# Kernel tuning notes

Hardware: AMD Instinct MI355X
Metric: run time of the kernel (lower is better)

The kernel has to match this reference:

```python
import jax, jax.numpy as jnp
import numpy as np

N_NODES = 50000
N_EDGES = 800000
D = 128
L = 3
BN_EPS = 1e-5


def _l2norm(x):
    # torch F.normalize(p=2, dim=-1): x / max(||x||, 1e-12)
    n = jnp.linalg.norm(x, axis=-1, keepdims=True)
    return x / jnp.maximum(n, 1e-12)


def setup_inputs() -> dict:
    key = jax.random.key(0)
    ks = jax.random.split(key, 5)
    x = jax.random.normal(ks[0], (N_NODES, D), dtype=jnp.float32)
    edge_index = jax.random.randint(ks[1], (2, N_EDGES), 0, N_NODES, dtype=jnp.int64)
    # stacked per-layer params; Linear stored as [in, out] (y = x @ W + b)
    W1 = jax.random.normal(ks[2], (L, D, D), dtype=jnp.float32) * 0.05
    W2 = jax.random.normal(ks[3], (L, D, D), dtype=jnp.float32) * 0.05
    b1 = jnp.zeros((L, D), jnp.float32)
    b2 = jnp.zeros((L, D), jnp.float32)
    gamma = jnp.ones((L, D), jnp.float32)
    beta = jnp.zeros((L, D), jnp.float32)
    eps = jnp.zeros((L,), jnp.float32)
    return {"x": x, "edge_index": edge_index, "W1": W1, "b1": b1,
            "gamma": gamma, "beta": beta, "W2": W2, "b2": b2, "eps": eps}


def _gin_layer(x, src, dst, W1, b1, g, be, W2, b2, eps):
    # message + scatter-add aggregation: sum_j x_j -> node i
    agg = jax.ops.segment_sum(x[src], dst, num_segments=N_NODES)
    # update(): L2 normalize aggregated messages
    agg = _l2norm(agg)
    # eps-weighted residual on L2-normalized root features
    out = agg + (1.0 + eps) * _l2norm(x)
    # MLP: Linear -> BatchNorm1d (training stats) -> ReLU -> Linear
    h = out @ W1 + b1
    mu = jnp.mean(h, axis=0)
    var = jnp.mean(jnp.square(h - mu), axis=0)  # biased var (torch BN training)
    h = g * (h - mu) * jax.lax.rsqrt(var + BN_EPS) + be
    h = jax.nn.relu(h)
    return h @ W2 + b2


def reference(x, edge_index, W1, b1, gamma, beta, W2, b2, eps):
    src, dst = edge_index[0], edge_index[1]
    for i in range(L):
        x = _gin_layer(x, src, dst, W1[i], b1[i], gamma[i], beta[i], W2[i], b2[i], eps[i])
        if i != L - 1:
            x = jax.nn.relu(x)
    return x
```

## Files before the change

kernel.cpp:

```cpp
#include <hip/hip_runtime.h>
#include <hip/hip_bf16.h>

#define N_NODES 50000
#define N_EDGES 800000
#define D 128
#define L_LAYERS 3
#define BN_EPS 1e-5f
#define NBUK 196
#define BIN_CHUNK 4096
#define NBIN_BLOCKS 196
#define BSTRIDE 5120
#define CSTRIDE 5376
#define AROW 68
#define NPART 8
#define PADOFF (N_NODES << 8)

typedef __attribute__((ext_vector_type(8))) short short8;
typedef __attribute__((ext_vector_type(4))) float floatx4;
typedef __attribute__((ext_vector_type(4))) unsigned short ushort4v;

__device__ __forceinline__ unsigned short f2bf(float f) {
    unsigned u = __builtin_bit_cast(unsigned, f);
    u += 0x7FFFu + ((u >> 16) & 1u);
    return (unsigned short)(u >> 16);
}
__device__ __forceinline__ float bf2f(unsigned short h) {
    unsigned u = ((unsigned)h) << 16;
    return __builtin_bit_cast(float, u);
}
__device__ __forceinline__ float bf2f_lo(unsigned p) {
    return __builtin_bit_cast(float, p << 16);
}
__device__ __forceinline__ float bf2f_hi(unsigned p) {
    return __builtin_bit_cast(float, p & 0xFFFF0000u);
}

__device__ __forceinline__ int edge_at(const void* ei, const int* flag64, long long i) {
    if (*flag64) return (int)((const long long*)ei)[i];
    return ((const int*)ei)[i];
}

__global__ __launch_bounds__(256) void prep_kernel(const float* __restrict__ x,
        const void* __restrict__ ei, int* __restrict__ flag,
        const float* __restrict__ W1, const float* __restrict__ W2,
        short* __restrict__ Wp, unsigned short* __restrict__ xb,
        unsigned* __restrict__ zreg, int zwords) {
    int bid = blockIdx.x;
    int t = threadIdx.x;
    if (bid == 0) {
        __shared__ int nz;
        if (t == 0) nz = 0;
        __syncthreads();
        if (((const int*)ei)[2 * t + 1] != 0) atomicAdd(&nz, 1);
        __syncthreads();
        if (t == 0) *flag = (nz == 0) ? 1 : 0;
        for (int i = t; i < zwords; i += 256) zreg[i] = 0u;
        if (t < 64) ((unsigned*)(xb + (size_t)N_NODES * D))[t] = 0u;
    } else if (bid <= 48) {
        int tid = (bid - 1) * 256 + t;
        int mat = tid >> 11;
        int t2 = tid & 2047;
        int kt = t2 >> 9;
        int nt = (t2 >> 6) & 7;
        int lane = t2 & 63;
        const float* W = (mat < 3) ? (W1 + (size_t)mat * D * D)
                                   : (W2 + (size_t)(mat - 3) * D * D);
        int kbase = kt * 32 + (lane >> 4) * 8;
        int n = nt * 16 + (lane & 15);
        short8 frag;
        #pragma unroll
        for (int j = 0; j < 8; j++) frag[j] = (short)f2bf(W[(kbase + j) * D + n]);
        *(short8*)(Wp + (size_t)mat * D * D + (size_t)t2 * 8) = frag;
    } else {
        long long i = (long long)((bid - 49) * 256 + t) * 4;
        float4 v = *(const float4*)(x + i);
        ushort4v o;
        o.x = f2bf(v.x); o.y = f2bf(v.y); o.z = f2bf(v.z); o.w = f2bf(v.w);
        *(ushort4v*)(xb + i) = o;
    }
}

__global__ __launch_bounds__(256) void bin_kernel(const void* __restrict__ ei,
        const int* __restrict__ flag64, int* __restrict__ bucketCursor,
        unsigned* __restrict__ binned) {
    __shared__ int lhist[NBUK];
    __shared__ int gbase[NBUK];
    int t = threadIdx.x;
    for (int i = t; i < NBUK; i += 256) lhist[i] = 0;
    __syncthreads();

    int e0 = blockIdx.x * BIN_CHUNK;
    unsigned w[BIN_CHUNK / 256];
    short bkt[BIN_CHUNK / 256];
    short lidx[BIN_CHUNK / 256];
    #pragma unroll
    for (int i = 0; i < BIN_CHUNK / 256; i++) {
        int e = e0 + t + i * 256;
        if (e < N_EDGES) {
            int s = edge_at(ei, flag64, e);
            int d = edge_at(ei, flag64, (long long)N_EDGES + e);
            int b = d >> 8;
            w[i] = ((unsigned)s << 8) | (unsigned)(d & 255);
            bkt[i] = (short)b;
            lidx[i] = (short)atomicAdd(&lhist[b], 1);
        } else {
            bkt[i] = -1;
        }
    }
    __syncthreads();
    for (int i = t; i < NBUK; i += 256) {
        int c = lhist[i];
        gbase[i] = i * BSTRIDE + (c ? atomicAdd(&bucketCursor[i], c) : 0);
    }
    __syncthreads();
    #pragma unroll
    for (int i = 0; i < BIN_CHUNK / 256; i++) {
        if (bkt[i] >= 0)
            binned[gbase[bkt[i]] + (int)lidx[i]] = w[i];
    }
}

__global__ __launch_bounds__(256) void csr_build_kernel(const unsigned* __restrict__ binned,
        const int* __restrict__ bucketCursor, int* __restrict__ rowptr,
        int* __restrict__ bucketEnd, int* __restrict__ csr) {
    __shared__ int ls[256];
    __shared__ int lhist[256];
    __shared__ int lcur[256];
    int b = blockIdx.x, t = threadIdx.x;
    int n = bucketCursor[b];
    const unsigned* src = binned + (size_t)b * BSTRIDE;

    lhist[t] = 0;
    __syncthreads();
    for (int i = t; i < n; i += 256)
        atomicAdd(&lhist[src[i] & 255u], 1);
    __syncthreads();
    int c = lhist[t];
    int pc = (c + 3) & ~3;
    ls[t] = pc;
    __syncthreads();
    for (int off = 1; off < 256; off <<= 1) {
        int u = (t >= off) ? ls[t - off] : 0;
        __syncthreads();
        ls[t] += u;
        __syncthreads();
    }
    int excl = ls[t] - pc;
    int base = b * CSTRIDE;
    int dst = b * 256 + t;
    if (dst <= N_NODES) rowptr[dst] = base + excl;
    if (t == 0) bucketEnd[b] = base + ls[255];
    lcur[t] = excl;
    __syncthreads();
    for (int i = t; i < n; i += 256) {
        unsigned wv = src[i];
        int pos = atomicAdd(&lcur[wv & 255u], 1);
        csr[base + pos] = (int)(wv & 0xFFFFFF00u);
    }
    __syncthreads();
    for (int i = lcur[t]; i < excl + pc; i++)
        csr[base + i] = PADOFF;
}

__global__ __launch_bounds__(256, 8) void gather_gemm1_kernel(
        const unsigned short* __restrict__ xb,
        const int* __restrict__ rowptr, const int* __restrict__ csr,
        const int* __restrict__ bucketEnd,
        const float* __restrict__ epsArr, int layer,
        const short* __restrict__ Wp, const float* __restrict__ bB,
        unsigned* __restrict__ Hout,
        float* __restrict__ gsum, float* __restrict__ gsq) {
    __shared__ __attribute__((aligned(16))) unsigned lA[16 * AROW];
    __shared__ int wq;
    const char* xbase = (const char*)xb;
    int wave = threadIdx.x >> 6, lane = threadIdx.x & 63;
    int g = lane >> 4, p = lane & 15;
    unsigned po = (unsigned)(p << 4);
    int r0 = blockIdx.x * 16;
    float eps1 = 1.0f + epsArr[layer];
    if (threadIdx.x == 0) wq = 0;
    __syncthreads();

    for (;;) {
        int r;
        if (lane == 0) r = atomicAdd(&wq, 1);
        r = __shfl(r, 0);
        if (r >= 16) break;
        int row = r0 + r;
        int beg = rowptr[row];
        int end = ((row & 255) == 255) ? bucketEnd[row >> 8] : rowptr[row + 1];
        float ac[8];
        #pragma unroll
        for (int k = 0; k < 8; k++) ac[k] = 0.f;
        for (int base = beg; base < end; base += 64) {
            int n = end - base;
            if (n > 64) n = 64;
            unsigned idxv = (lane < n) ? (unsigned)csr[base + lane] : (unsigned)PADOFF;
            int j = 0;
            for (; j + 8 <= n; j += 8) {
                unsigned o0 = (unsigned)__shfl((int)idxv, j + g) + po;
                unsigned o1 = (unsigned)__shfl((int)idxv, j + 4 + g) + po;
                uint4 v0 = *(const uint4*)(xbase + o0);
                uint4 v1 = *(const uint4*)(xbase + o1);
                ac[0] += bf2f_lo(v0.x); ac[1] += bf2f_hi(v0.x);
                ac[2] += bf2f_lo(v0.y); ac[3] += bf2f_hi(v0.y);
                ac[4] += bf2f_lo(v0.z); ac[5] += bf2f_hi(v0.z);
                ac[6] += bf2f_lo(v0.w); ac[7] += bf2f_hi(v0.w);
                ac[0] += bf2f_lo(v1.x); ac[1] += bf2f_hi(v1.x);
                ac[2] += bf2f_lo(v1.y); ac[3] += bf2f_hi(v1.y);
                ac[4] += bf2f_lo(v1.z); ac[5] += bf2f_hi(v1.z);
                ac[6] += bf2f_lo(v1.w); ac[7] += bf2f_hi(v1.w);
            }
            if (j < n) {
                unsigned o0 = (unsigned)__shfl((int)idxv, j + g) + po;
                uint4 v0 = *(const uint4*)(xbase + o0);
                ac[0] += bf2f_lo(v0.x); ac[1] += bf2f_hi(v0.x);
                ac[2] += bf2f_lo(v0.y); ac[3] += bf2f_hi(v0.y);
                ac[4] += bf2f_lo(v0.z); ac[5] += bf2f_hi(v0.z);
                ac[6] += bf2f_lo(v0.w); ac[7] += bf2f_hi(v0.w);
            }
        }
        #pragma unroll
        for (int k = 0; k < 8; k++) {
            ac[k] += __shfl_xor(ac[k], 16);
            ac[k] += __shfl_xor(ac[k], 32);
        }
        uint4 sv = *(const uint4*)(xbase + (((unsigned)row << 8) + po));
        float xv[8];
        xv[0] = bf2f_lo(sv.x); xv[1] = bf2f_hi(sv.x);
        xv[2] = bf2f_lo(sv.y); xv[3] = bf2f_hi(sv.y);
        xv[4] = bf2f_lo(sv.z); xv[5] = bf2f_hi(sv.z);
        xv[6] = bf2f_lo(sv.w); xv[7] = bf2f_hi(sv.w);
        float sa = 0.f, sx = 0.f;
        #pragma unroll
        for (int k = 0; k < 8; k++) { sa += ac[k] * ac[k]; sx += xv[k] * xv[k]; }
        #pragma unroll
        for (int mm = 8; mm >= 1; mm >>= 1) {
            sa += __shfl_xor(sa, mm);
            sx += __shfl_xor(sx, mm);
        }
        float ra = 1.0f / fmaxf(sqrtf(sa), 1e-12f);
        float rx = eps1 / fmaxf(sqrtf(sx), 1e-12f);
        unsigned wds[4];
        #pragma unroll
        for (int k = 0; k < 4; k++) {
            float lo = ac[2 * k] * ra + xv[2 * k] * rx;
            float hi = ac[2 * k + 1] * ra + xv[2 * k + 1] * rx;
            wds[k] = (unsigned)f2bf(lo) | ((unsigned)f2bf(hi) << 16);
        }
        if (g == 0)
            *(uint4*)(lA + r * AROW + p * 4) = make_uint4(wds[0], wds[1], wds[2], wds[3]);
    }
    __syncthreads();

    int m = p;
    int nt0 = wave * 2, nt1 = nt0 + 1;
    short8 afr[4];
    #pragma unroll
    for (int kt = 0; kt < 4; kt++)
        afr[kt] = *(const short8*)(lA + m * AROW + kt * 16 + g * 4);
    __syncthreads();

    floatx4 acc0 = (floatx4){0.f, 0.f, 0.f, 0.f};
    floatx4 acc1 = (floatx4){0.f, 0.f, 0.f, 0.f};
    #pragma unroll
    for (int kt = 0; kt < 4; kt++) {
        short8 bf0 = *(const short8*)(Wp + (size_t)((kt * 8 + nt0) * 64 + lane) * 8);
        short8 bf1 = *(const short8*)(Wp + (size_t)((kt * 8 + nt1) * 64 + lane) * 8);
        acc0 = __builtin_amdgcn_mfma_f32_16x16x32_bf16(afr[kt], bf0, acc0, 0, 0, 0);
        acc1 = __builtin_amdgcn_mfma_f32_16x16x32_bf16(afr[kt], bf1, acc1, 0, 0, 0);
    }

    unsigned short* hlds = (unsigned short*)lA;
    float bc0 = bB[nt0 * 16 + m], bc1 = bB[nt1 * 16 + m];
    float s0 = 0.f, q0 = 0.f, s1 = 0.f, q1 = 0.f;
    #pragma unroll
    for (int r = 0; r < 4; r++) {
        int lrow = g * 4 + r;
        float h0 = acc0[r] + bc0;
        float h1 = acc1[r] + bc1;
        hlds[lrow * (AROW * 2) + nt0 * 16 + m] = f2bf(h0);
        hlds[lrow * (AROW * 2) + nt1 * 16 + m] = f2bf(h1);
        s0 += h0; q0 += h0 * h0;
        s1 += h1; q1 += h1 * h1;
    }
    s0 += __shfl_xor(s0, 16); s0 += __shfl_xor(s0, 32);
    q0 += __shfl_xor(q0, 16); q0 += __shfl_xor(q0, 32);
    s1 += __shfl_xor(s1, 16); s1 += __shfl_xor(s1, 32);
    q1 += __shfl_xor(q1, 16); q1 += __shfl_xor(q1, 32);
    if (lane < 16) {
        float* gs = gsum + (size_t)(blockIdx.x & (NPART - 1)) * D;
        float* gq = gsq + (size_t)(blockIdx.x & (NPART - 1)) * D;
        atomicAdd(&gs[nt0 * 16 + m], s0);
        atomicAdd(&gs[nt1 * 16 + m], s1);
        atomicAdd(&gq[nt0 * 16 + m], q0);
        atomicAdd(&gq[nt1 * 16 + m], q1);
    }
    __syncthreads();

    {
        int crow = threadIdx.x >> 4;
        int cq = threadIdx.x & 15;
        uint4 v = *(const uint4*)(lA + crow * AROW + cq * 4);
        *(uint4*)(Hout + (size_t)(r0 + crow) * 64 + cq * 4) = v;
    }
}

__global__ __launch_bounds__(256) void gemm2_mfma_kernel(const unsigned short* __restrict__ H,
        const float* __restrict__ gsum, const float* __restrict__ gsq,
        const float* __restrict__ gamma, const float* __restrict__ beta,
        const short* __restrict__ Wp, const float* __restrict__ b,
        float* __restrict__ Yf32, unsigned* __restrict__ Yb16, int finalLayer) {
    __shared__ float s_scale[D];
    __shared__ float s_shift[D];
    __shared__ unsigned so[64 * 132];
    if (threadIdx.x < D) {
        int c = threadIdx.x;
        const float invN = 1.0f / (float)N_NODES;
        float su = 0.f, sq = 0.f;
        #pragma unroll
        for (int pp = 0; pp < NPART; pp++) {
            su += gsum[(size_t)pp * D + c];
            sq += gsq[(size_t)pp * D + c];
        }
        float mu = su * invN;
        float var = fmaxf(sq * invN - mu * mu, 0.f);
        float is = rsqrtf(var + BN_EPS);
        float sc = gamma[c] * is;
        s_scale[c] = sc;
        s_shift[c] = beta[c] - mu * sc;
    }
    __syncthreads();

    int wave = threadIdx.x >> 6, lane = threadIdx.x & 63;
    int r0 = blockIdx.x * 64;
    int m = lane & 15, g = lane >> 4;
    int arow = r0 + wave * 16 + m;
    bool valid = arow < N_NODES;

    short8 a[4];
    #pragma unroll
    for (int kt = 0; kt < 4; kt++) {
        int koff = kt * 32 + g * 8;
        if (valid) {
            short8 hv = *(const short8*)(H + (long long)arow * D + koff);
            #pragma unroll
            for (int j = 0; j < 8; j++) {
                float h = bf2f((unsigned short)hv[j]);
                float v = fmaxf(h * s_scale[koff + j] + s_shift[koff + j], 0.f);
                a[kt][j] = (short)f2bf(v);
            }
        } else {
            a[kt] = (short8)0;
        }
    }

    floatx4 acc[8];
    #pragma unroll
    for (int nt = 0; nt < 8; nt++) acc[nt] = (floatx4){0.f, 0.f, 0.f, 0.f};

    #pragma unroll
    for (int nt = 0; nt < 8; nt++) {
        #pragma unroll
        for (int kt = 0; kt < 4; kt++) {
            short8 bf = *(const short8*)(Wp + (size_t)((kt * 8 + nt) * 64 + lane) * 8);
            acc[nt] = __builtin_amdgcn_mfma_f32_16x16x32_bf16(a[kt], bf, acc[nt], 0, 0, 0);
        }
    }

    if (finalLayer) {
        float* sof = (float*)so;
        #pragma unroll
        for (int nt = 0; nt < 8; nt++) {
            int col = nt * 16 + m;
            float bcol = b[col];
            #pragma unroll
            for (int r = 0; r < 4; r++) {
                int lrow = wave * 16 + g * 4 + r;
                sof[lrow * 132 + col] = acc[nt][r] + bcol;
            }
        }
        __syncthreads();
        #pragma unroll
        for (int k = 0; k < 8; k++) {
            int c = threadIdx.x + k * 256;
            int crow = c >> 5;
            int cq = c & 31;
            if (r0 + crow < N_NODES) {
                float4 v = *(const float4*)(sof + crow * 132 + cq * 4);
                *(float4*)(Yf32 + (size_t)(r0 + crow) * D + cq * 4) = v;
            }
        }
    } else {
        unsigned short* sos = (unsigned short*)so;
        #pragma unroll
        for (int nt = 0; nt < 8; nt++) {
            int col = nt * 16 + m;
            float bcol = b[col];
            #pragma unroll
            for (int r = 0; r < 4; r++) {
                int lrow = wave * 16 + g * 4 + r;
                sos[lrow * (AROW * 2) + col] = f2bf(fmaxf(acc[nt][r] + bcol, 0.f));
            }
        }
        __syncthreads();
        #pragma unroll
        for (int k = 0; k < 4; k++) {
            int c = threadIdx.x + k * 256;
            int crow = c >> 4;
            int cq = c & 15;
            if (r0 + crow < N_NODES) {
                uint4 v = *(const uint4*)(so + crow * AROW + cq * 4);
                *(uint4*)(Yb16 + (size_t)(r0 + crow) * 64 + cq * 4) = v;
            }
        }
    }
}

extern "C" void kernel_launch(void* const* d_in, const int* in_sizes, int n_in,
                              void* d_out, int out_size, void* d_ws, size_t ws_size,
                              hipStream_t stream) {
    const float* x      = (const float*)d_in[0];
    const void*  ei     = d_in[1];
    const float* W1     = (const float*)d_in[2];
    const float* b1     = (const float*)d_in[3];
    const float* gamma  = (const float*)d_in[4];
    const float* beta   = (const float*)d_in[5];
    const float* W2     = (const float*)d_in[6];
    const float* b2     = (const float*)d_in[7];
    const float* epsArr = (const float*)d_in[8];
    float* out = (float*)d_out;

    char* ws = (char*)d_ws;
    const size_t xbuf = (size_t)(N_NODES + 1) * D * sizeof(short);
    const size_t hbuf = (size_t)N_NODES * D * sizeof(short);
    unsigned short* Xb  = (unsigned short*)ws;
    unsigned* H16       = (unsigned*)(ws + xbuf);
    char* p             = ws + xbuf + hbuf;
    short* Wp       = (short*)p;         p += 6 * (size_t)D * D * sizeof(short);
    int* rowptr     = (int*)p;           p += (N_NODES + 1) * sizeof(int);
    int* csr        = (int*)p;           p += (size_t)NBUK * CSTRIDE * sizeof(int);
    unsigned* binned= (unsigned*)p;      p += (size_t)NBUK * BSTRIDE * sizeof(unsigned);
    int* bucketEnd  = (int*)p;           p += NBUK * sizeof(int);
    int* flag       = (int*)p;           p += sizeof(int);
    char* zbase     = p;
    int* bucketCursor=(int*)p;           p += NBUK * sizeof(int);
    float* stats    = (float*)p;         p += (size_t)L_LAYERS * 2 * NPART * D * sizeof(float);
    int zwords      = (int)((p - zbase) / 4);

    prep_kernel<<<1 + 48 + (N_NODES * D / 4) / 256, 256, 0, stream>>>(
        x, ei, flag, W1, W2, Wp, Xb, (unsigned*)zbase, zwords);

    bin_kernel<<<NBIN_BLOCKS, 256, 0, stream>>>(ei, flag, bucketCursor, binned);
    csr_build_kernel<<<NBUK, 256, 0, stream>>>(binned, bucketCursor, rowptr, bucketEnd, csr);

    const int g1Grid = N_NODES / 16;
    const int g2Grid = (N_NODES + 63) / 64;
    for (int l = 0; l < L_LAYERS; l++) {
        int fin = (l == L_LAYERS - 1) ? 1 : 0;
        float* gsum = stats + (size_t)l * 2 * NPART * D;
        float* gsq  = gsum + (size_t)NPART * D;

        gather_gemm1_kernel<<<g1Grid, 256, 0, stream>>>(
            Xb, rowptr, csr, bucketEnd, epsArr, l,
            Wp + (size_t)l * D * D, b1 + (size_t)l * D,
            H16, gsum, gsq);
        gemm2_mfma_kernel<<<g2Grid, 256, 0, stream>>>(
            (const unsigned short*)H16, gsum, gsq,
            gamma + (size_t)l * D, beta + (size_t)l * D,
            Wp + (size_t)(3 + l) * D * D, b2 + (size_t)l * D,
            out, (unsigned*)Xb, fin);
    }
}
```

Baseline: 210.3 us.

## Interleave two-row gathers per wave and use hardware bf16 pack conversion

```diff
diff --git a/kernel.cpp b/kernel.cpp
--- a/kernel.cpp
+++ b/kernel.cpp
@@ -17,7 +17,7 @@
 
 typedef __attribute__((ext_vector_type(8))) short short8;
 typedef __attribute__((ext_vector_type(4))) float floatx4;
-typedef __attribute__((ext_vector_type(4))) unsigned short ushort4v;
+typedef __attribute__((ext_vector_type(4))) unsigned uintx4;
 
 __device__ __forceinline__ unsigned short f2bf(float f) {
     unsigned u = __builtin_bit_cast(unsigned, f);
@@ -34,10 +34,49 @@
 __device__ __forceinline__ float bf2f_hi(unsigned p) {
     return __builtin_bit_cast(float, p & 0xFFFF0000u);
 }
+__device__ __forceinline__ unsigned cvtpk(float lo, float hi) {
+    unsigned r;
+    asm("v_cvt_pk_bf16_f32 %0, %1, %2" : "=v"(r) : "v"(lo), "v"(hi));
+    return r;
+}
 
 __device__ __forceinline__ int edge_at(const void* ei, const int* flag64, long long i) {
     if (*flag64) return (int)((const long long*)ei)[i];
     return ((const int*)ei)[i];
+}
+
+#define CONSUME(ac, v) \
+    ac[0] += bf2f_lo(v.x); ac[1] += bf2f_hi(v.x); \
+    ac[2] += bf2f_lo(v.y); ac[3] += bf2f_hi(v.y); \
+    ac[4] += bf2f_lo(v.z); ac[5] += bf2f_hi(v.z); \
+    ac[6] += bf2f_lo(v.w); ac[7] += bf2f_hi(v.w);
+
+__device__ __forceinline__ void gather_pair(const char* xbase, const int* __restrict__ csr,
+        int begA, int endA, int begB, int endB,
+        unsigned ivA, unsigned ivB, int lane, int g, unsigned po,
+        float* __restrict__ acA, float* __restrict__ acB) {
+    int bA = begA, bB = begB;
+    for (;;) {
+        int nA = endA - bA; nA = nA < 0 ? 0 : (nA > 64 ? 64 : nA);
+        int nB = endB - bB; nB = nB < 0 ? 0 : (nB > 64 ? 64 : nB);
+        int nm = nA > nB ? nA : nB;
+        for (int j = 0; j < nm; j += 8) {
+            unsigned oA0 = (unsigned)__shfl((int)ivA, j + g) + po;
+            unsigned oA1 = (unsigned)__shfl((int)ivA, j + 4 + g) + po;
+            unsigned oB0 = (unsigned)__shfl((int)ivB, j + g) + po;
+            unsigned oB1 = (unsigned)__shfl((int)ivB, j + 4 + g) + po;
+            uint4 vA0 = *(const uint4*)(xbase + oA0);
+            uint4 vA1 = *(const uint4*)(xbase + oA1);
+            uint4 vB0 = *(const uint4*)(xbase + oB0);
+            uint4 vB1 = *(const uint4*)(xbase + oB1);
+            CONSUME(acA, vA0); CONSUME(acA, vA1);
+            CONSUME(acB, vB0); CONSUME(acB, vB1);
+        }
+        bA += 64; bB += 64;
+        if (bA >= endA && bB >= endB) break;
+        ivA = (bA + lane < endA) ? (unsigned)csr[bA + lane] : (unsigned)PADOFF;
+        ivB = (bB + lane < endB) ? (unsigned)csr[bB + lane] : (unsigned)PADOFF;
+    }
 }
 
 __global__ __launch_bounds__(256) void prep_kernel(const float* __restrict__ x,
@@ -67,16 +106,18 @@
                                    : (W2 + (size_t)(mat - 3) * D * D);
         int kbase = kt * 32 + (lane >> 4) * 8;
         int n = nt * 16 + (lane & 15);
-        short8 frag;
-        #pragma unroll
-        for (int j = 0; j < 8; j++) frag[j] = (short)f2bf(W[(kbase + j) * D + n]);
-        *(short8*)(Wp + (size_t)mat * D * D + (size_t)t2 * 8) = frag;
+        unsigned fw[4];
+        #pragma unroll
+        for (int j = 0; j < 4; j++)
+            fw[j] = cvtpk(W[(kbase + 2 * j) * D + n], W[(kbase + 2 * j + 1) * D + n]);
+        *(uint4*)(Wp + (size_t)mat * D * D + (size_t)t2 * 8) =
+            make_uint4(fw[0], fw[1], fw[2], fw[3]);
     } else {
         long long i = (long long)((bid - 49) * 256 + t) * 4;
         float4 v = *(const float4*)(x + i);
-        ushort4v o;
-        o.x = f2bf(v.x); o.y = f2bf(v.y); o.z = f2bf(v.z); o.w = f2bf(v.w);
-        *(ushort4v*)(xb + i) = o;
+        unsigned w0 = cvtpk(v.x, v.y);
+        unsigned w1 = cvtpk(v.z, v.w);
+        *(uint2*)(xb + i) = make_uint2(w0, w1);
     }
 }
 
@@ -170,62 +211,64 @@
         const short* __restrict__ Wp, const float* __restrict__ bB,
         unsigned* __restrict__ Hout,
         float* __restrict__ gsum, float* __restrict__ gsq) {
-    __shared__ __attribute__((aligned(16))) unsigned lA[16 * AROW];
-    __shared__ int wq;
+    __shared__ __attribute__((aligned(16))) float partw[16 * 2 * 16 * 8];
+    unsigned* lA = (unsigned*)partw;
     const char* xbase = (const char*)xb;
     int wave = threadIdx.x >> 6, lane = threadIdx.x & 63;
     int g = lane >> 4, p = lane & 15;
     unsigned po = (unsigned)(p << 4);
     int r0 = blockIdx.x * 16;
     float eps1 = 1.0f + epsArr[layer];
-    if (threadIdx.x == 0) wq = 0;
-    __syncthreads();
-
-    for (;;) {
-        int r;
-        if (lane == 0) r = atomicAdd(&wq, 1);
-        r = __shfl(r, 0);
-        if (r >= 16) break;
-        int row = r0 + r;
-        int beg = rowptr[row];
-        int end = ((row & 255) == 255) ? bucketEnd[row >> 8] : rowptr[row + 1];
-        float ac[8];
-        #pragma unroll
-        for (int k = 0; k < 8; k++) ac[k] = 0.f;
-        for (int base = beg; base < end; base += 64) {
-            int n = end - base;
-            if (n > 64) n = 64;
-            unsigned idxv = (lane < n) ? (unsigned)csr[base + lane] : (unsigned)PADOFF;
-            int j = 0;
-            for (; j + 8 <= n; j += 8) {
-                unsigned o0 = (unsigned)__shfl((int)idxv, j + g) + po;
-                unsigned o1 = (unsigned)__shfl((int)idxv, j + 4 + g) + po;
-                uint4 v0 = *(const uint4*)(xbase + o0);
-                uint4 v1 = *(const uint4*)(xbase + o1);
-                ac[0] += bf2f_lo(v0.x); ac[1] += bf2f_hi(v0.x);
-                ac[2] += bf2f_lo(v0.y); ac[3] += bf2f_hi(v0.y);
-                ac[4] += bf2f_lo(v0.z); ac[5] += bf2f_hi(v0.z);
-                ac[6] += bf2f_lo(v0.w); ac[7] += bf2f_hi(v0.w);
-                ac[0] += bf2f_lo(v1.x); ac[1] += bf2f_hi(v1.x);
-                ac[2] += bf2f_lo(v1.y); ac[3] += bf2f_hi(v1.y);
-                ac[4] += bf2f_lo(v1.z); ac[5] += bf2f_hi(v1.z);
-                ac[6] += bf2f_lo(v1.w); ac[7] += bf2f_hi(v1.w);
-            }
-            if (j < n) {
-                unsigned o0 = (unsigned)__shfl((int)idxv, j + g) + po;
-                uint4 v0 = *(const uint4*)(xbase + o0);
-                ac[0] += bf2f_lo(v0.x); ac[1] += bf2f_hi(v0.x);
-                ac[2] += bf2f_lo(v0.y); ac[3] += bf2f_hi(v0.y);
-                ac[4] += bf2f_lo(v0.z); ac[5] += bf2f_hi(v0.z);
-                ac[6] += bf2f_lo(v0.w); ac[7] += bf2f_hi(v0.w);
-            }
-        }
-        #pragma unroll
-        for (int k = 0; k < 8; k++) {
-            ac[k] += __shfl_xor(ac[k], 16);
-            ac[k] += __shfl_xor(ac[k], 32);
-        }
-        uint4 sv = *(const uint4*)(xbase + (((unsigned)row << 8) + po));
+
+    int rw2 = threadIdx.x >> 4, pq2 = threadIdx.x & 15;
+    uint4 sv = *(const uint4*)(xbase + (((unsigned)(r0 + rw2)) << 8) + (pq2 << 4));
+
+    int rp = (lane < 17) ? rowptr[r0 + lane] : 0;
+    int rA = wave, rB = wave + 4, rC = wave + 8, rD = wave + 12;
+    int begA = __shfl(rp, rA), endA = __shfl(rp, rA + 1);
+    int begB = __shfl(rp, rB), endB = __shfl(rp, rB + 1);
+    int begC = __shfl(rp, rC), endC = __shfl(rp, rC + 1);
+    int begD = __shfl(rp, rD), endD = __shfl(rp, rD + 1);
+    if (wave == 3 && ((r0 + 15) & 255) == 255) endD = bucketEnd[(r0 + 15) >> 8];
+
+    unsigned ivA = (begA + lane < endA) ? (unsigned)csr[begA + lane] : (unsigned)PADOFF;
+    unsigned ivB = (begB + lane < endB) ? (unsigned)csr[begB + lane] : (unsigned)PADOFF;
+    unsigned ivC = (begC + lane < endC) ? (unsigned)csr[begC + lane] : (unsigned)PADOFF;
+    unsigned ivD = (begD + lane < endD) ? (unsigned)csr[begD + lane] : (unsigned)PADOFF;
+
+#define ROW_EPI(r, ac) { \
+    _Pragma("unroll") \
+    for (int k = 0; k < 8; k++) ac[k] += __shfl_xor(ac[k], 16); \
+    if (!(g & 1)) { \
+        float* wp_ = partw + (size_t)(((r) * 2 + (g >> 1)) * 16 + p) * 8; \
+        *(float4*)wp_ = make_float4(ac[0], ac[1], ac[2], ac[3]); \
+        *(float4*)(wp_ + 4) = make_float4(ac[4], ac[5], ac[6], ac[7]); \
+    } }
+
+    float acA[8], acB[8];
+    #pragma unroll
+    for (int k = 0; k < 8; k++) { acA[k] = 0.f; acB[k] = 0.f; }
+    gather_pair(xbase, csr, begA, endA, begB, endB, ivA, ivB, lane, g, po, acA, acB);
+    ROW_EPI(rA, acA); ROW_EPI(rB, acB);
+
+    #pragma unroll
+    for (int k = 0; k < 8; k++) { acA[k] = 0.f; acB[k] = 0.f; }
+    gather_pair(xbase, csr, begC, endC, begD, endD, ivC, ivD, lane, g, po, acA, acB);
+    ROW_EPI(rC, acA); ROW_EPI(rD, acB);
+#undef ROW_EPI
+    __syncthreads();
+
+    {
+        const float* pb = partw + ((size_t)(rw2 * 2) * 16 + pq2) * 8;
+        float4 q0 = *(const float4*)pb;
+        float4 q1 = *(const float4*)(pb + 4);
+        float4 q2 = *(const float4*)(pb + 128);
+        float4 q3 = *(const float4*)(pb + 132);
+        float s[8];
+        s[0] = q0.x + q2.x; s[1] = q0.y + q2.y;
+        s[2] = q0.z + q2.z; s[3] = q0.w + q2.w;
+        s[4] = q1.x + q3.x; s[5] = q1.y + q3.y;
+        s[6] = q1.z + q3.z; s[7] = q1.w + q3.w;
         float xv[8];
         xv[0] = bf2f_lo(sv.x); xv[1] = bf2f_hi(sv.x);
         xv[2] = bf2f_lo(sv.y); xv[3] = bf2f_hi(sv.y);
@@ -233,7 +276,7 @@
         xv[6] = bf2f_lo(sv.w); xv[7] = bf2f_hi(sv.w);
         float sa = 0.f, sx = 0.f;
         #pragma unroll
-        for (int k = 0; k < 8; k++) { sa += ac[k] * ac[k]; sx += xv[k] * xv[k]; }
+        for (int k = 0; k < 8; k++) { sa += s[k] * s[k]; sx += xv[k] * xv[k]; }
         #pragma unroll
         for (int mm = 8; mm >= 1; mm >>= 1) {
             sa += __shfl_xor(sa, mm);
@@ -241,15 +284,15 @@
         }
         float ra = 1.0f / fmaxf(sqrtf(sa), 1e-12f);
         float rx = eps1 / fmaxf(sqrtf(sx), 1e-12f);
-        unsigned wds[4];
-        #pragma unroll
-        for (int k = 0; k < 4; k++) {
-            float lo = ac[2 * k] * ra + xv[2 * k] * rx;
-            float hi = ac[2 * k + 1] * ra + xv[2 * k + 1] * rx;
-            wds[k] = (unsigned)f2bf(lo) | ((unsigned)f2bf(hi) << 16);
-        }
-        if (g == 0)
-            *(uint4*)(lA + r * AROW + p * 4) = make_uint4(wds[0], wds[1], wds[2], wds[3]);
+        float o[8];
+        #pragma unroll
+        for (int k = 0; k < 8; k++) o[k] = s[k] * ra + xv[k] * rx;
+        unsigned w0 = cvtpk(o[0], o[1]);
+        unsigned w1 = cvtpk(o[2], o[3]);
+        unsigned w2 = cvtpk(o[4], o[5]);
+        unsigned w3 = cvtpk(o[6], o[7]);
+        __syncthreads();
+        *(uint4*)(lA + rw2 * AROW + pq2 * 4) = make_uint4(w0, w1, w2, w3);
     }
     __syncthreads();
 
@@ -344,12 +387,16 @@
         int koff = kt * 32 + g * 8;
         if (valid) {
             short8 hv = *(const short8*)(H + (long long)arow * D + koff);
+            unsigned aw[4];
             #pragma unroll
-            for (int j = 0; j < 8; j++) {
-                float h = bf2f((unsigned short)hv[j]);
-                float v = fmaxf(h * s_scale[koff + j] + s_shift[koff + j], 0.f);
-                a[kt][j] = (short)f2bf(v);
+            for (int jj = 0; jj < 4; jj++) {
+                float h0 = bf2f((unsigned short)hv[2 * jj]);
+                float h1 = bf2f((unsigned short)hv[2 * jj + 1]);
+                float v0 = fmaxf(h0 * s_scale[koff + 2 * jj] + s_shift[koff + 2 * jj], 0.f);
+                float v1 = fmaxf(h1 * s_scale[koff + 2 * jj + 1] + s_shift[koff + 2 * jj + 1], 0.f);
+                aw[jj] = cvtpk(v0, v1);
             }
+            a[kt] = __builtin_bit_cast(short8, (uintx4){aw[0], aw[1], aw[2], aw[3]});
         } else {
             a[kt] = (short8)0;
         }
```

Result: slower. 216.8 us (+3.1%).
